# Performance work log

Hardware: AMD Instinct MI355X
Metric: run time of the kernel (lower is better)

The kernel has to match this reference:

```python
import jax, jax.numpy as jnp
import numpy as np


def setup_inputs() -> dict:
    key = jax.random.key(0)
    k1, k2, k3, k4, k5, k6 = jax.random.split(key, 6)
    H = 1024
    B, La, Lq = 32, 512, 64
    # kaiming_uniform with a=sqrt(5) on [H,H]: bound = sqrt(6/((1+5)*H)) = 1/sqrt(H)
    bound = 1.0 / np.sqrt(H)
    return {
        "article_feature": jax.random.normal(k1, (B, La, H), dtype=jnp.float32),
        "query_op_feature": jax.random.normal(k2, (B, Lq, H), dtype=jnp.float32),
        "weight1_1": jax.random.uniform(k3, (H, H), minval=-bound, maxval=bound, dtype=jnp.float32),
        "weight1_2": jax.random.uniform(k4, (H, H), minval=-bound, maxval=bound, dtype=jnp.float32),
        "weight2_1": jax.random.uniform(k5, (H, H), minval=-bound, maxval=bound, dtype=jnp.float32),
        "weight2_2": jax.random.uniform(k6, (H, H), minval=-bound, maxval=bound, dtype=jnp.float32),
    }


def reference(article_feature, query_op_feature, weight1_1, weight1_2, weight2_1, weight2_2):
    # article_feature: [B, La, H], query_op_feature: [B, Lq, H]
    # aq_attention: softmax over Lq of (A @ W1_1) @ Q^T -> [B, La, Lq]
    aq_scores = jnp.einsum("bah,hk,bqk->baq", article_feature, weight1_1, query_op_feature)
    aq_attention = jax.nn.softmax(aq_scores, axis=2)
    # qa_attention: softmax over La of (Q @ W1_2) @ A^T -> [B, Lq, La]
    qa_scores = jnp.einsum("bqh,hk,bak->bqa", query_op_feature, weight1_2, article_feature)
    qa_attention = jax.nn.softmax(qa_scores, axis=2)
    # S_a: relu((aq_attention @ Q) @ W2_1) -> [B, La, H]
    S_a = jax.nn.relu(jnp.einsum("baq,bqh,hk->bak", aq_attention, query_op_feature, weight2_1))
    # S_q: relu((qa_attention @ A) @ W2_2) -> [B, Lq, H]
    S_q = jax.nn.relu(jnp.einsum("bqa,bah,hk->bqk", qa_attention, article_feature, weight2_2))
    S_aq = jnp.max(S_a, axis=1)  # [B, H]
    S_qa = jnp.max(S_q, axis=1)  # [B, H]
    g = jnp.float32(0.5)
    return g * S_aq + (1.0 - g) * S_qa
```

## Files before the change

### kernel.cpp

```cpp
#include <hip/hip_runtime.h>
#include <stdint.h>


using f16x8 = __attribute__((ext_vector_type(8))) _Float16;
using f32x4 = __attribute__((ext_vector_type(4))) float;
typedef const __attribute__((address_space(1))) void* gas_t;
typedef __attribute__((address_space(3))) void* las_t;

__device__ __forceinline__ unsigned short f2h(float x) {
  _Float16 h = (_Float16)x;
  return __builtin_bit_cast(unsigned short, h);
}


__global__ __launch_bounds__(256) void prep_all(
    const float* __restrict__ W11, const float* __restrict__ W12,
    const float* __restrict__ W21, const float* __restrict__ W22,
    const float* __restrict__ Qfeat,
    unsigned short* __restrict__ Wcat, unsigned short* __restrict__ W21T,
    unsigned short* __restrict__ W22T, unsigned short* __restrict__ Q_hi)
{
  int z = blockIdx.z;
  int tx = threadIdx.x, ty = threadIdx.y;
  if (z >= 4) {
    int blk = (z - 4) * 1024 + blockIdx.y * 32 + blockIdx.x;
    int i = blk * 256 + ty * 32 + tx;
    float4 v = ((const float4*)Qfeat)[i];
    ushort4 h;
    h.x = f2h(v.x); h.y = f2h(v.y); h.z = f2h(v.z); h.w = f2h(v.w);
    ((ushort4*)Q_hi)[i] = h;
    return;
  }
  __shared__ float tile[32][33];
  const float* src = z == 0 ? W11 : z == 1 ? W12 : z == 2 ? W21 : W22;
  int r0 = blockIdx.y * 32, c0 = blockIdx.x * 32;
  #pragma unroll
  for (int i = 0; i < 4; ++i) {
    int r = r0 + ty + i * 8;
    float v = src[(long)r * 1024 + c0 + tx];
    tile[ty + i * 8][tx] = v;
    if (z == 0) Wcat[(long)r * 1024 + c0 + tx] = f2h(v);
  }
  __syncthreads();
  if (z > 0) {
    #pragma unroll
    for (int i = 0; i < 4; ++i) {
      float v = tile[tx][ty + i * 8];
      long o = (long)(c0 + ty + i * 8) * 1024 + r0 + tx;
      if (z == 1)      Wcat[1048576 + o] = f2h(v);
      else if (z == 2) W21T[o] = f2h(v);
      else             W22T[o] = f2h(v);
    }
  }
}

template<int BM, int BN, int OUT, bool BF32>
__device__ __forceinline__ void gemm_body(
    char* smem, int bx, int by, int z,
    const unsigned short* __restrict__ Ah,
    const unsigned short* __restrict__ Bh, const float* __restrict__ Bf,
    float* __restrict__ Cf, unsigned short* __restrict__ Ch,
    int M, int N, int K, int ldA, int ldB, int ldC, long sA, long sB, long sC)
{
  constexpr int ACH = BM * 64, BCH = BN * 64;
  constexpr int MI = BM / 32, NI = BN / 32;
  char* As0 = smem;
  char* As1 = smem + ACH;
  char* Bs0 = smem + 2 * ACH;
  char* Bs1 = Bs0 + BCH;

  const int m0 = by * BM, n0 = bx * BN;
  const int t = threadIdx.x, lane = t & 63;
  const int wid = t >> 6, wr = wid >> 1, wc = wid & 1;

  const unsigned short* Ab = Ah + (long)z * sA;
  const unsigned short* Bb = BF32 ? nullptr : Bh + (long)z * sB;
  const float* Bfb = BF32 ? Bf + (long)z * sB : nullptr;

  f32x4 acc[MI][NI];
  #pragma unroll
  for (int i = 0; i < MI; ++i)
    #pragma unroll
    for (int j = 0; j < NI; ++j)
      acc[i][j] = f32x4{0.f, 0.f, 0.f, 0.f};

  auto stage4k = [&](char* lbuf, const unsigned short* g, int ld, int row0, int k0, int rmax) {
    int ob = t * 16;
    int e  = ob ^ (((ob >> 7) & 3) << 4);
    int m  = e >> 6, k = (e & 63) >> 1;
    int row = row0 + m; row = row < rmax ? row : rmax - 1;
    const unsigned short* gp = g + (long)row * ld + k0 + k;
    char* lp = lbuf + (t & ~63) * 16;
    __builtin_amdgcn_global_load_lds((gas_t)(const void*)gp, (las_t)(void*)lp, 16, 0, 0);
  };
  auto stageB_f32 = [&](char* lbuf, const float* g, int ld, int nb, int k0) {
    int ob = t * 16;
    int e  = ob ^ (((ob >> 7) & 3) << 4);
    int n  = e >> 6, kb = (e & 63) >> 1;
    f16x8 pk;
    #pragma unroll
    for (int j = 0; j < 8; ++j) {
      float v = g[(long)(k0 + kb + j) * ld + nb + n];
      pk[j] = (_Float16)v;
    }
    *(f16x8*)(lbuf + ob) = pk;
  };
  auto ldfrag = [&](const char* lbuf, int rr) -> f16x8 {
    int ob = rr * 64 + (lane >> 4) * 16;
    ob ^= ((ob >> 7) & 3) << 4;
    return *(const f16x8*)(lbuf + ob);
  };
  auto compute32 = [&](const char* Ac, const char* Bc) {
    f16x8 ah[MI];
    #pragma unroll
    for (int mi = 0; mi < MI; ++mi)
      ah[mi] = ldfrag(Ac, wr * (BM / 2) + mi * 16 + (lane & 15));
    #pragma unroll
    for (int ni = 0; ni < NI; ++ni) {
      f16x8 bh = ldfrag(Bc, wc * (BN / 2) + ni * 16 + (lane & 15));
      #pragma unroll
      for (int mi = 0; mi < MI; ++mi)
        acc[mi][ni] = __builtin_amdgcn_mfma_f32_16x16x32_f16(ah[mi], bh, acc[mi][ni], 0, 0, 0);
    }
  };

  for (int k0 = 0; k0 < K; k0 += 64) {
    stage4k(As0, Ab, ldA, m0, k0, M);
    if (BM == 128) stage4k(As0 + 4096, Ab, ldA, m0 + 64, k0, M);
    stage4k(As1, Ab, ldA, m0, k0 + 32, M);
    if (BM == 128) stage4k(As1 + 4096, Ab, ldA, m0 + 64, k0 + 32, M);
    if (BF32) {
      stageB_f32(Bs0, Bfb, ldB, n0, k0);
      stageB_f32(Bs1, Bfb, ldB, n0, k0 + 32);
    } else {
      stage4k(Bs0, Bb, ldB, n0, k0, N);
      stage4k(Bs1, Bb, ldB, n0, k0 + 32, N);
    }
    __syncthreads();
    compute32(As0, Bs0);
    compute32(As1, Bs1);
    __syncthreads();
  }

  if (OUT == 6) {
    float* red = (float*)smem;
    #pragma unroll
    for (int ni = 0; ni < NI; ++ni) {
      float pm = 0.0f;
      #pragma unroll
      for (int mi = 0; mi < MI; ++mi)
        #pragma unroll
        for (int r = 0; r < 4; ++r)
          pm = fmaxf(pm, acc[mi][ni][r]);
      int g = wr * 4 + (lane >> 4);
      int col = wc * (BN / 2) + ni * 16 + (lane & 15);
      red[g * BN + col] = pm;
    }
    __syncthreads();
    if (t < BN) {
      float pq = red[t];
      #pragma unroll
      for (int g = 1; g < 8; ++g) pq = fmaxf(pq, red[g * BN + t]);
      float pa = Bf[(long)(by * 4) * 1024 + n0 + t];
      #pragma unroll
      for (int mt = 1; mt < 4; ++mt)
        pa = fmaxf(pa, Bf[(long)(by * 4 + mt) * 1024 + n0 + t]);
      Cf[(long)by * 1024 + n0 + t] = 0.5f * pa + 0.5f * pq;
    }
    return;
  }

  #pragma unroll
  for (int mi = 0; mi < MI; ++mi) {
    #pragma unroll
    for (int r = 0; r < 4; ++r) {
      int grow = m0 + wr * (BM / 2) + mi * 16 + (lane >> 4) * 4 + r;
      #pragma unroll
      for (int ni = 0; ni < NI; ++ni) {
        int gcol = n0 + wc * (BN / 2) + ni * 16 + (lane & 15);
        float v = acc[mi][ni][r];
        if (OUT == 1) {
          int b = grow >> 6, q = grow & 63;
          long dst = (long)b * 131072 + (long)((gcol >> 10) * 64 + q) * 1024 + (gcol & 1023);
          Ch[dst] = f2h(v);
        } else if (OUT == 2) {
          if (grow < M) Ch[(long)z * sC + (long)grow * ldC + gcol] = f2h(v);
        } else if (OUT == 3) {
          long dst = (long)(grow >> 6) * 65536 + (long)gcol * 64 + (grow & 63);
          Ch[dst] = f2h(v);
        }
      }
    }
  }
}


__global__ __launch_bounds__(256) void g1_kernel(
    const unsigned short* Q_hi, const unsigned short* Wcat, const unsigned short* W21T,
    unsigned short* Pcat, unsigned short* P3T)
{
  __shared__ char smem[24576];
  int bid = blockIdx.x;
  if (bid < 512) {
    gemm_body<128, 64, 1, false>(smem, bid & 31, bid >> 5, 0,
        Q_hi, Wcat, nullptr, nullptr, Pcat,
        2048, 2048, 1024, 1024, 1024, 0, 0, 0, 0);
  } else {
    int b2 = bid - 512;
    gemm_body<128, 64, 3, false>(smem, b2 & 15, b2 >> 4, 0,
        Q_hi, W21T, nullptr, nullptr, P3T,
        2048, 1024, 1024, 1024, 1024, 0, 0, 0, 0);
  }
}


__global__ __launch_bounds__(512) void g2_kernel(
    const float* __restrict__ Afeat, const unsigned short* __restrict__ Pcat,
    unsigned short* __restrict__ aq, float* __restrict__ Spar)
{
  __shared__ char smem[20480];
  char* A0 = smem;
  char* A1 = smem + 2048;
  char* B0 = smem + 4096;
  char* B1 = smem + 12288;

  int orig = blockIdx.x;
  int xcd = orig & 7, idx = orig >> 3;
  int z   = xcd * 4 + (idx >> 4);
  int mt  = idx & 15;
  const int m0 = mt * 32;
  const int t = threadIdx.x, lane = t & 63;
  const int wid = t >> 6, wr = wid >> 2, wc = wid & 3;

  const float* Ab = Afeat + (long)z * 524288;
  const unsigned short* Bb = Pcat + (long)z * 131072;

  f32x4 acc[2];
  acc[0] = f32x4{0.f, 0.f, 0.f, 0.f};
  acc[1] = f32x4{0.f, 0.f, 0.f, 0.f};

  auto ldfrag = [&](const char* lbuf, int rr) -> f16x8 {
    int ob = rr * 64 + (lane >> 4) * 16;
    ob ^= ((ob >> 7) & 3) << 4;
    return *(const f16x8*)(lbuf + ob);
  };
  auto stageA = [&](int k0) {
    int half = t >> 8, tt = t & 255;
    int ob = tt * 8;
    int e  = ob ^ (((ob >> 7) & 3) << 4);
    int m  = e >> 6, ke = (e & 63) >> 1;
    float4 v = *(const float4*)(Ab + (long)(m0 + m) * 1024 + k0 + half * 32 + ke);
    ushort4 h;
    h.x = f2h(v.x); h.y = f2h(v.y); h.z = f2h(v.z); h.w = f2h(v.w);
    *(ushort4*)((half ? A1 : A0) + ob) = h;
  };
  auto stageB = [&](char* lbuf, int k0) {
    int ob = t * 16;
    int e  = ob ^ (((ob >> 7) & 3) << 4);
    int n  = e >> 6, kk = (e & 63) >> 1;
    const unsigned short* gp = Bb + (long)n * 1024 + k0 + kk;
    char* lp = lbuf + (t & ~63) * 16;
    __builtin_amdgcn_global_load_lds((gas_t)(const void*)gp, (las_t)(void*)lp, 16, 0, 0);
  };
  auto compute32 = [&](const char* Ac, const char* Bc) {
    f16x8 ah = ldfrag(Ac, wr * 16 + (lane & 15));
    #pragma unroll
    for (int ni = 0; ni < 2; ++ni) {
      f16x8 bh = ldfrag(Bc, wc * 32 + ni * 16 + (lane & 15));
      acc[ni] = __builtin_amdgcn_mfma_f32_16x16x32_f16(ah, bh, acc[ni], 0, 0, 0);
    }
  };

  for (int k0 = 0; k0 < 1024; k0 += 64) {
    stageA(k0);
    stageB(B0, k0);
    stageB(B1, k0 + 32);
    __syncthreads();
    compute32(A0, B0);
    compute32(A1, B1);
    __syncthreads();
  }

  float* red = (float*)smem;
  #pragma unroll
  for (int ni = 0; ni < 2; ++ni)
    #pragma unroll
    for (int r = 0; r < 4; ++r) {
      int lrow = wr * 16 + (lane >> 4) * 4 + r;
      int col  = wc * 32 + ni * 16 + (lane & 15);
      red[lrow * 128 + col] = acc[ni][r];
    }
  __syncthreads();

  int row = t >> 4, cg = (t & 15) * 4;
  float a0 = red[row * 128 + cg],     a1 = red[row * 128 + cg + 1];
  float a2 = red[row * 128 + cg + 2], a3 = red[row * 128 + cg + 3];
  float4 vq = *(float4*)&red[row * 128 + 64 + cg];
  float mx = fmaxf(fmaxf(a0, a1), fmaxf(a2, a3));
  #pragma unroll
  for (int off = 8; off; off >>= 1) mx = fmaxf(mx, __shfl_xor(mx, off));
  float e0 = __expf(a0 - mx), e1 = __expf(a1 - mx);
  float e2 = __expf(a2 - mx), e3 = __expf(a3 - mx);
  float s = (e0 + e1) + (e2 + e3);
  #pragma unroll
  for (int off = 8; off; off >>= 1) s += __shfl_xor(s, off);
  float inv = 1.0f / s;
  ushort4 h;
  h.x = f2h(e0 * inv); h.y = f2h(e1 * inv); h.z = f2h(e2 * inv); h.w = f2h(e3 * inv);
  long base = (long)z * 32768 + (long)(m0 + row) * 64 + cg;
  *(ushort4*)(aq + base) = h;
  *(float4*)(Spar + base) = vq;
}


__global__ __launch_bounds__(256) void softmax_cols(const float* __restrict__ Sp,
                                                    unsigned short* __restrict__ qa)
{
  int bq = blockIdx.x;
  int b = bq >> 6, q = bq & 63;
  int t = threadIdx.x;
  const float* base = Sp + (long)b * 32768 + q;
  float v0 = base[(long)t * 64];
  float v1 = base[(long)(t + 256) * 64];
  float m = fmaxf(v0, v1);
  #pragma unroll
  for (int off = 32; off; off >>= 1) m = fmaxf(m, __shfl_xor(m, off));
  __shared__ float sm[4], ss[4];
  int wid = t >> 6, lane = t & 63;
  if (lane == 0) sm[wid] = m;
  __syncthreads();
  float M = fmaxf(fmaxf(sm[0], sm[1]), fmaxf(sm[2], sm[3]));
  float e0 = __expf(v0 - M), e1 = __expf(v1 - M);
  float s = e0 + e1;
  #pragma unroll
  for (int off = 32; off; off >>= 1) s += __shfl_xor(s, off);
  if (lane == 0) ss[wid] = s;
  __syncthreads();
  float inv = 1.0f / ((ss[0] + ss[1]) + (ss[2] + ss[3]));
  qa[(long)bq * 512 + t]       = f2h(e0 * inv);
  qa[(long)bq * 512 + t + 256] = f2h(e1 * inv);
}


__global__ __launch_bounds__(256) void g3_kernel(
    const unsigned short* aq, const unsigned short* P3T, float* PmaxA,
    const unsigned short* qa, const float* Afeat, unsigned short* ctx)
{
  __shared__ char smem[16384];
  int bid = blockIdx.x;
  if (bid < 1024) {
    int bx = bid & 7, by = (bid >> 3) & 3, z = bid >> 5;
    int n0 = bx * 128, m0 = by * 128;
    const unsigned short* Aq = aq + (long)z * 32768;
    const unsigned short* Bp = P3T + (long)z * 65536;
    const int t = threadIdx.x, lane = t & 63;
    const int wid = t >> 6, wr = wid >> 1, wc = wid & 1;

    f32x4 acc[4][4];
    #pragma unroll
    for (int i = 0; i < 4; ++i)
      #pragma unroll
      for (int j = 0; j < 4; ++j)
        acc[i][j] = f32x4{0.f, 0.f, 0.f, 0.f};

    #pragma unroll
    for (int c = 0; c < 2; ++c) {
      f16x8 ah[4];
      #pragma unroll
      for (int mi = 0; mi < 4; ++mi) {
        int row = m0 + wr * 64 + mi * 16 + (lane & 15);
        ah[mi] = *(const f16x8*)(Aq + (long)row * 64 + c * 32 + (lane >> 4) * 8);
      }
      #pragma unroll
      for (int ni = 0; ni < 4; ++ni) {
        int rc = n0 + wc * 64 + ni * 16 + (lane & 15);
        f16x8 bh = *(const f16x8*)(Bp + (long)rc * 64 + c * 32 + (lane >> 4) * 8);
        #pragma unroll
        for (int mi = 0; mi < 4; ++mi)
          acc[mi][ni] = __builtin_amdgcn_mfma_f32_16x16x32_f16(ah[mi], bh, acc[mi][ni], 0, 0, 0);
      }
    }

    float* red = (float*)smem;
    #pragma unroll
    for (int ni = 0; ni < 4; ++ni) {
      float pm = 0.0f;
      #pragma unroll
      for (int mi = 0; mi < 4; ++mi)
        #pragma unroll
        for (int r = 0; r < 4; ++r)
          pm = fmaxf(pm, acc[mi][ni][r]);
      int g = wr * 4 + (lane >> 4);
      int col = wc * 64 + ni * 16 + (lane & 15);
      red[g * 128 + col] = pm;
    }
    __syncthreads();
    if (t < 128) {
      float m = red[t];
      #pragma unroll
      for (int g = 1; g < 8; ++g) m = fmaxf(m, red[g * 128 + t]);
      PmaxA[(long)(z * 4 + by) * 1024 + n0 + t] = m;
    }
  } else {
    int b2 = bid - 1024;
    gemm_body<64, 64, 2, true>(smem, b2 & 15, 0, b2 >> 4,
        qa, nullptr, Afeat, nullptr, ctx,
        64, 1024, 512, 512, 1024, 1024, 32768L, 524288L, 65536L);
  }
}


__global__ __launch_bounds__(256) void g4_kernel(
    const unsigned short* ctx, const unsigned short* W22T,
    const float* PmaxA, float* out)
{
  __shared__ char smem[16384];
  gemm_body<64, 64, 6, false>(smem, blockIdx.x, blockIdx.y, 0,
      ctx, W22T, PmaxA, out, nullptr,
      2048, 1024, 1024, 1024, 1024, 1024, 0, 0, 0);
}


extern "C" void kernel_launch(void* const* d_in, const int* in_sizes, int n_in,
                              void* d_out, int out_size, void* d_ws, size_t ws_size,
                              hipStream_t stream) {
  const float* Afeat = (const float*)d_in[0];
  const float* Qfeat = (const float*)d_in[1];
  const float* W11   = (const float*)d_in[2];
  const float* W12   = (const float*)d_in[3];
  const float* W21   = (const float*)d_in[4];
  const float* W22   = (const float*)d_in[5];
  float* out = (float*)d_out;

  char* w = (char*)d_ws;
  auto alloc = [&](long bytes) { char* p = w; w += bytes; return p; };
  unsigned short* Q_hi  = (unsigned short*)alloc(4194304);
  unsigned short* Wcat  = (unsigned short*)alloc(4194304);
  unsigned short* W21T  = (unsigned short*)alloc(2097152);
  unsigned short* W22T  = (unsigned short*)alloc(2097152);
  unsigned short* Pcat  = (unsigned short*)alloc(8388608);
  unsigned short* P3T   = (unsigned short*)alloc(4194304);
  float*          Spar  = (float*)alloc(4194304);
  unsigned short* aq    = (unsigned short*)alloc(2097152);
  unsigned short* qa    = (unsigned short*)alloc(2097152);
  unsigned short* ctx   = (unsigned short*)alloc(4194304);
  float*          PmaxA = (float*)alloc(524288);

  dim3 blk(256), tblk(32, 8);

  prep_all<<<dim3(32, 32, 6), tblk, 0, stream>>>(W11, W12, W21, W22, Qfeat,
                                                 Wcat, W21T, W22T, Q_hi);
  g1_kernel<<<768, blk, 0, stream>>>(Q_hi, Wcat, W21T, Pcat, P3T);
  g2_kernel<<<512, dim3(512), 0, stream>>>(Afeat, Pcat, aq, Spar);
  softmax_cols<<<2048, blk, 0, stream>>>(Spar, qa);
  g3_kernel<<<1536, blk, 0, stream>>>(aq, P3T, PmaxA, qa, Afeat, ctx);
  g4_kernel<<<dim3(16, 32), blk, 0, stream>>>(ctx, W22T, PmaxA, out);
}
```

Before: 95.85 us.

## Fuse column softmax into the ctx GEMM and write qa scores transposed

g2 now writes the qa scores transposed (SparT, [B, Lq, La]), so each query row is contiguous. The separate softmax_cols kernel is removed and its work moves into the ctx branch of g3: each block computes row max and sum over 512 entries, then builds the normalized fp16 qa tiles on the fly while staging. The ctx GEMM tile becomes 64x128 with 256 blocks instead of 64x64 with 512, which saves one launch and the qa round trip through memory. In exchange, the exponentials are recomputed in every block (8 column blocks per batch), g2 now does strided scalar stores, and fewer blocks run the ctx path.

```diff
diff --git a/kernel.cpp b/kernel.cpp
--- a/kernel.cpp
+++ b/kernel.cpp
@@ -54,12 +54,11 @@
   }
 }
 
-template<int BM, int BN, int OUT, bool BF32>
+template<int BM, int BN, int OUT>
 __device__ __forceinline__ void gemm_body(
     char* smem, int bx, int by, int z,
-    const unsigned short* __restrict__ Ah,
-    const unsigned short* __restrict__ Bh, const float* __restrict__ Bf,
-    float* __restrict__ Cf, unsigned short* __restrict__ Ch,
+    const unsigned short* __restrict__ Ah, const unsigned short* __restrict__ Bh,
+    const float* __restrict__ Bf, float* __restrict__ Cf, unsigned short* __restrict__ Ch,
     int M, int N, int K, int ldA, int ldB, int ldC, long sA, long sB, long sC)
 {
   constexpr int ACH = BM * 64, BCH = BN * 64;
@@ -74,8 +73,7 @@
   const int wid = t >> 6, wr = wid >> 1, wc = wid & 1;
 
   const unsigned short* Ab = Ah + (long)z * sA;
-  const unsigned short* Bb = BF32 ? nullptr : Bh + (long)z * sB;
-  const float* Bfb = BF32 ? Bf + (long)z * sB : nullptr;
+  const unsigned short* Bb = Bh + (long)z * sB;
 
   f32x4 acc[MI][NI];
   #pragma unroll
@@ -93,18 +91,6 @@
     char* lp = lbuf + (t & ~63) * 16;
     __builtin_amdgcn_global_load_lds((gas_t)(const void*)gp, (las_t)(void*)lp, 16, 0, 0);
   };
-  auto stageB_f32 = [&](char* lbuf, const float* g, int ld, int nb, int k0) {
-    int ob = t * 16;
-    int e  = ob ^ (((ob >> 7) & 3) << 4);
-    int n  = e >> 6, kb = (e & 63) >> 1;
-    f16x8 pk;
-    #pragma unroll
-    for (int j = 0; j < 8; ++j) {
-      float v = g[(long)(k0 + kb + j) * ld + nb + n];
-      pk[j] = (_Float16)v;
-    }
-    *(f16x8*)(lbuf + ob) = pk;
-  };
   auto ldfrag = [&](const char* lbuf, int rr) -> f16x8 {
     int ob = rr * 64 + (lane >> 4) * 16;
     ob ^= ((ob >> 7) & 3) << 4;
@@ -129,13 +115,8 @@
     if (BM == 128) stage4k(As0 + 4096, Ab, ldA, m0 + 64, k0, M);
     stage4k(As1, Ab, ldA, m0, k0 + 32, M);
     if (BM == 128) stage4k(As1 + 4096, Ab, ldA, m0 + 64, k0 + 32, M);
-    if (BF32) {
-      stageB_f32(Bs0, Bfb, ldB, n0, k0);
-      stageB_f32(Bs1, Bfb, ldB, n0, k0 + 32);
-    } else {
-      stage4k(Bs0, Bb, ldB, n0, k0, N);
-      stage4k(Bs1, Bb, ldB, n0, k0 + 32, N);
-    }
+    stage4k(Bs0, Bb, ldB, n0, k0, N);
+    stage4k(Bs1, Bb, ldB, n0, k0 + 32, N);
     __syncthreads();
     compute32(As0, Bs0);
     compute32(As1, Bs1);
@@ -183,8 +164,6 @@
           int b = grow >> 6, q = grow & 63;
           long dst = (long)b * 131072 + (long)((gcol >> 10) * 64 + q) * 1024 + (gcol & 1023);
           Ch[dst] = f2h(v);
-        } else if (OUT == 2) {
-          if (grow < M) Ch[(long)z * sC + (long)grow * ldC + gcol] = f2h(v);
         } else if (OUT == 3) {
           long dst = (long)(grow >> 6) * 65536 + (long)gcol * 64 + (grow & 63);
           Ch[dst] = f2h(v);
@@ -202,12 +181,12 @@
   __shared__ char smem[24576];
   int bid = blockIdx.x;
   if (bid < 512) {
-    gemm_body<128, 64, 1, false>(smem, bid & 31, bid >> 5, 0,
+    gemm_body<128, 64, 1>(smem, bid & 31, bid >> 5, 0,
         Q_hi, Wcat, nullptr, nullptr, Pcat,
         2048, 2048, 1024, 1024, 1024, 0, 0, 0, 0);
   } else {
     int b2 = bid - 512;
-    gemm_body<128, 64, 3, false>(smem, b2 & 15, b2 >> 4, 0,
+    gemm_body<128, 64, 3>(smem, b2 & 15, b2 >> 4, 0,
         Q_hi, W21T, nullptr, nullptr, P3T,
         2048, 1024, 1024, 1024, 1024, 0, 0, 0, 0);
   }
@@ -216,7 +195,7 @@
 
 __global__ __launch_bounds__(512) void g2_kernel(
     const float* __restrict__ Afeat, const unsigned short* __restrict__ Pcat,
-    unsigned short* __restrict__ aq, float* __restrict__ Spar)
+    unsigned short* __restrict__ aq, float* __restrict__ SparT)
 {
   __shared__ char smem[20480];
   char* A0 = smem;
@@ -309,51 +288,28 @@
   h.x = f2h(e0 * inv); h.y = f2h(e1 * inv); h.z = f2h(e2 * inv); h.w = f2h(e3 * inv);
   long base = (long)z * 32768 + (long)(m0 + row) * 64 + cg;
   *(ushort4*)(aq + base) = h;
-  *(float4*)(Spar + base) = vq;
-}
-
-
-__global__ __launch_bounds__(256) void softmax_cols(const float* __restrict__ Sp,
-                                                    unsigned short* __restrict__ qa)
+  long tb = (long)z * 32768 + (long)(m0 + row);
+  SparT[tb + (long)(cg + 0) * 512] = vq.x;
+  SparT[tb + (long)(cg + 1) * 512] = vq.y;
+  SparT[tb + (long)(cg + 2) * 512] = vq.z;
+  SparT[tb + (long)(cg + 3) * 512] = vq.w;
+}
+
+
+__global__ __launch_bounds__(256) void g3_kernel(
+    const unsigned short* __restrict__ aq, const unsigned short* __restrict__ P3T,
+    float* __restrict__ PmaxA,
+    const float* __restrict__ SparT, const float* __restrict__ Afeat,
+    unsigned short* __restrict__ ctx)
 {
-  int bq = blockIdx.x;
-  int b = bq >> 6, q = bq & 63;
-  int t = threadIdx.x;
-  const float* base = Sp + (long)b * 32768 + q;
-  float v0 = base[(long)t * 64];
-  float v1 = base[(long)(t + 256) * 64];
-  float m = fmaxf(v0, v1);
-  #pragma unroll
-  for (int off = 32; off; off >>= 1) m = fmaxf(m, __shfl_xor(m, off));
-  __shared__ float sm[4], ss[4];
-  int wid = t >> 6, lane = t & 63;
-  if (lane == 0) sm[wid] = m;
-  __syncthreads();
-  float M = fmaxf(fmaxf(sm[0], sm[1]), fmaxf(sm[2], sm[3]));
-  float e0 = __expf(v0 - M), e1 = __expf(v1 - M);
-  float s = e0 + e1;
-  #pragma unroll
-  for (int off = 32; off; off >>= 1) s += __shfl_xor(s, off);
-  if (lane == 0) ss[wid] = s;
-  __syncthreads();
-  float inv = 1.0f / ((ss[0] + ss[1]) + (ss[2] + ss[3]));
-  qa[(long)bq * 512 + t]       = f2h(e0 * inv);
-  qa[(long)bq * 512 + t + 256] = f2h(e1 * inv);
-}
-
-
-__global__ __launch_bounds__(256) void g3_kernel(
-    const unsigned short* aq, const unsigned short* P3T, float* PmaxA,
-    const unsigned short* qa, const float* Afeat, unsigned short* ctx)
-{
-  __shared__ char smem[16384];
+  __shared__ char smem[25088];
   int bid = blockIdx.x;
+  const int t = threadIdx.x, lane = t & 63;
   if (bid < 1024) {
     int bx = bid & 7, by = (bid >> 3) & 3, z = bid >> 5;
     int n0 = bx * 128, m0 = by * 128;
     const unsigned short* Aq = aq + (long)z * 32768;
     const unsigned short* Bp = P3T + (long)z * 65536;
-    const int t = threadIdx.x, lane = t & 63;
     const int wid = t >> 6, wr = wid >> 1, wc = wid & 1;
 
     f32x4 acc[4][4];
@@ -401,12 +357,116 @@
       for (int g = 1; g < 8; ++g) m = fmaxf(m, red[g * 128 + t]);
       PmaxA[(long)(z * 4 + by) * 1024 + n0 + t] = m;
     }
-  } else {
-    int b2 = bid - 1024;
-    gemm_body<64, 64, 2, true>(smem, b2 & 15, 0, b2 >> 4,
-        qa, nullptr, Afeat, nullptr, ctx,
-        64, 1024, 512, 512, 1024, 1024, 32768L, 524288L, 65536L);
-  }
+    return;
+  }
+
+  int b2 = bid - 1024;
+  int bx = b2 & 7, z = b2 >> 3;
+  const int n0 = bx * 128;
+  const float* S  = SparT + (long)z * 32768;
+  const float* Ab = Afeat + (long)z * 524288;
+  char* A0 = smem;
+  char* A1 = smem + 4096;
+  char* B0 = smem + 8192;
+  char* B1 = smem + 16384;
+  float* mxs  = (float*)(smem + 24576);
+  float* invs = mxs + 64;
+
+  {
+    int q = t >> 2, quarter = t & 3;
+    const float4* Sq = (const float4*)(S + q * 512 + quarter * 128);
+    float mx = -1e30f;
+    #pragma unroll 8
+    for (int i = 0; i < 32; ++i) {
+      float4 v = Sq[i];
+      mx = fmaxf(fmaxf(fmaxf(mx, v.x), fmaxf(v.y, v.z)), v.w);
+    }
+    mx = fmaxf(mx, __shfl_xor(mx, 1));
+    mx = fmaxf(mx, __shfl_xor(mx, 2));
+    float sum = 0.f;
+    #pragma unroll 8
+    for (int i = 0; i < 32; ++i) {
+      float4 v = Sq[i];
+      sum += (__expf(v.x - mx) + __expf(v.y - mx)) + (__expf(v.z - mx) + __expf(v.w - mx));
+    }
+    sum += __shfl_xor(sum, 1);
+    sum += __shfl_xor(sum, 2);
+    if (quarter == 0) { mxs[q] = mx; invs[q] = 1.0f / sum; }
+  }
+  __syncthreads();
+
+  const int wid = t >> 6, wr = wid >> 1, wc = wid & 1;
+  f32x4 acc[2][4];
+  #pragma unroll
+  for (int i = 0; i < 2; ++i)
+    #pragma unroll
+    for (int j = 0; j < 4; ++j)
+      acc[i][j] = f32x4{0.f, 0.f, 0.f, 0.f};
+
+  auto ldfrag = [&](const char* lbuf, int rr) -> f16x8 {
+    int ob = rr * 64 + (lane >> 4) * 16;
+    ob ^= ((ob >> 7) & 3) << 4;
+    return *(const f16x8*)(lbuf + ob);
+  };
+  auto stageQA = [&](char* lbuf, int k0) {
+    int ob = t * 16;
+    int e  = ob ^ (((ob >> 7) & 3) << 4);
+    int row = e >> 6, kb = (e & 63) >> 1;
+    const float* src = S + row * 512 + k0 + kb;
+    float m = mxs[row], inv = invs[row];
+    f16x8 pk;
+    #pragma unroll
+    for (int j = 0; j < 8; ++j) pk[j] = (_Float16)(__expf(src[j] - m) * inv);
+    *(f16x8*)(lbuf + ob) = pk;
+  };
+  auto stageBA = [&](char* lbuf, int nb, int k0) {
+    int ob = t * 16;
+    int e  = ob ^ (((ob >> 7) & 3) << 4);
+    int n  = e >> 6, kb = (e & 63) >> 1;
+    f16x8 pk;
+    #pragma unroll
+    for (int j = 0; j < 8; ++j)
+      pk[j] = (_Float16)Ab[(long)(k0 + kb + j) * 1024 + nb + n];
+    *(f16x8*)(lbuf + ob) = pk;
+  };
+  auto compute32 = [&](const char* Ac, const char* Bc) {
+    f16x8 ah[2];
+    #pragma unroll
+    for (int mi = 0; mi < 2; ++mi)
+      ah[mi] = ldfrag(Ac, wr * 32 + mi * 16 + (lane & 15));
+    #pragma unroll
+    for (int ni = 0; ni < 4; ++ni) {
+      f16x8 bh = ldfrag(Bc, wc * 64 + ni * 16 + (lane & 15));
+      #pragma unroll
+      for (int mi = 0; mi < 2; ++mi)
+        acc[mi][ni] = __builtin_amdgcn_mfma_f32_16x16x32_f16(ah[mi], bh, acc[mi][ni], 0, 0, 0);
+    }
+  };
+
+  for (int k0 = 0; k0 < 512; k0 += 64) {
+    stageQA(A0, k0);
+    stageQA(A1, k0 + 32);
+    stageBA(B0, n0, k0);
+    stageBA(B0 + 4096, n0 + 64, k0);
+    stageBA(B1, n0, k0 + 32);
+    stageBA(B1 + 4096, n0 + 64, k0 + 32);
+    __syncthreads();
+    compute32(A0, B0);
+    compute32(A1, B1);
+    __syncthreads();
+  }
+
+  #pragma unroll
+  for (int mi = 0; mi < 2; ++mi)
+    #pragma unroll
+    for (int r = 0; r < 4; ++r) {
+      int grow = wr * 32 + mi * 16 + (lane >> 4) * 4 + r;
+      #pragma unroll
+      for (int ni = 0; ni < 4; ++ni) {
+        int gcol = n0 + wc * 64 + ni * 16 + (lane & 15);
+        ctx[(long)z * 65536 + (long)grow * 1024 + gcol] = f2h(acc[mi][ni][r]);
+      }
+    }
 }
 
 
@@ -415,7 +475,7 @@
     const float* PmaxA, float* out)
 {
   __shared__ char smem[16384];
-  gemm_body<64, 64, 6, false>(smem, blockIdx.x, blockIdx.y, 0,
+  gemm_body<64, 64, 6>(smem, blockIdx.x, blockIdx.y, 0,
       ctx, W22T, PmaxA, out, nullptr,
       2048, 1024, 1024, 1024, 1024, 1024, 0, 0, 0);
 }
@@ -440,9 +500,8 @@
   unsigned short* W22T  = (unsigned short*)alloc(2097152);
   unsigned short* Pcat  = (unsigned short*)alloc(8388608);
   unsigned short* P3T   = (unsigned short*)alloc(4194304);
-  float*          Spar  = (float*)alloc(4194304);
+  float*          SparT = (float*)alloc(4194304);
   unsigned short* aq    = (unsigned short*)alloc(2097152);
-  unsigned short* qa    = (unsigned short*)alloc(2097152);
   unsigned short* ctx   = (unsigned short*)alloc(4194304);
   float*          PmaxA = (float*)alloc(524288);
 
@@ -451,8 +510,7 @@
   prep_all<<<dim3(32, 32, 6), tblk, 0, stream>>>(W11, W12, W21, W22, Qfeat,
                                                  Wcat, W21T, W22T, Q_hi);
   g1_kernel<<<768, blk, 0, stream>>>(Q_hi, Wcat, W21T, Pcat, P3T);
-  g2_kernel<<<512, dim3(512), 0, stream>>>(Afeat, Pcat, aq, Spar);
-  softmax_cols<<<2048, blk, 0, stream>>>(Spar, qa);
-  g3_kernel<<<1536, blk, 0, stream>>>(aq, P3T, PmaxA, qa, Afeat, ctx);
+  g2_kernel<<<512, dim3(512), 0, stream>>>(Afeat, Pcat, aq, SparT);
+  g3_kernel<<<1280, blk, 0, stream>>>(aq, P3T, PmaxA, SparT, Afeat, ctx);
   g4_kernel<<<dim3(16, 32), blk, 0, stream>>>(ctx, W22T, PmaxA, out);
 }
```

Result: slower. 120.3 us (+25.5%).
